# Performance work log

Hardware: AMD Instinct MI355X
Metric: run time of the kernel (lower is better)

Reference implementation:

```python
import jax, jax.numpy as jnp
import numpy as np

N = 8192       # number of points
C = 16         # num_colors (size of color distribution)
DIM = 2        # spatial dim (GeometricLoss(dim=2))


def setup_inputs() -> dict:
    key = jax.random.key(0)
    k1, k2 = jax.random.split(key)
    outputs = jax.random.normal(k1, (N, C), dtype=jnp.float32)
    points = jax.random.normal(k2, (N, DIM), dtype=jnp.float32)
    return {"outputs": outputs, "points": points, "k": 5}


def reference(outputs, points, k):
    # cdist(points, points) via the squared-norm expansion (avoids [N,N,dim] tensor)
    sq = jnp.sum(points * points, axis=1)                      # [N]
    d2 = sq[:, None] + sq[None, :] - 2.0 * (points @ points.T)  # [N,N]
    dist = jnp.sqrt(jnp.maximum(d2, 0.0))
    # k+1 smallest distances per row; drop self (distance 0)
    _, idx = jax.lax.top_k(-dist, k + 1)                        # [N,k+1]
    idx = idx[:, 1:]                                            # [N,k]
    neighbor_outputs = outputs[idx]                             # [N,k,C] gather
    # ||out_i - out_j|| over color dim, mean over all (i, neighbor) pairs
    differences = jnp.linalg.norm(outputs[:, None, :] - neighbor_outputs, axis=2)
    return differences.mean()
```

## Files before the change

### kernel.cpp

```cpp
#include <hip/hip_runtime.h>


static constexpr int NPTS = 8192;
static constexpr int KNN  = 5;
static constexpr int CH   = 16;
static constexpr int WPB  = 4;
static constexpr int NBLK = NPTS / WPB;
static constexpr int CAP  = 128;
static constexpr int NF4  = NPTS / 2;
static constexpr int BAT  = 8;
static constexpr int NBAT = NF4 / (64 * BAT);

__device__ __forceinline__ unsigned long long shfl_xor_u64(unsigned long long v, int m) {
    unsigned int lo = (unsigned int)v;
    unsigned int hi = (unsigned int)(v >> 32);
    lo = __shfl_xor(lo, m, 64);
    hi = __shfl_xor(hi, m, 64);
    return ((unsigned long long)hi << 32) | lo;
}

__global__ __launch_bounds__(256, 8) void knn_loss_kernel(
        const float* __restrict__ outputs,
        const float* __restrict__ points,
        float* __restrict__ partial) {
    const int wave = threadIdx.x >> 6;
    const int lane = threadIdx.x & 63;
    const int i = blockIdx.x * WPB + wave;

    const float2 pi = ((const float2*)points)[i];
    const float4* __restrict__ pts4 = (const float4*)points;
    const float FINF = __int_as_float(0x7f800000);

    float vA = FINF, vB = FINF;
    for (int b = 0; b < NBAT; ++b) {
        float4 p[BAT];
        #pragma unroll
        for (int q = 0; q < BAT; ++q)
            p[q] = pts4[b * (64 * BAT) + q * 64 + lane];
        #pragma unroll
        for (int q = 0; q < BAT; ++q) {
            const float dxa = pi.x - p[q].x, dya = pi.y - p[q].y;
            const float dxb = pi.x - p[q].z, dyb = pi.y - p[q].w;
            const float d2a = fmaf(dxa, dxa, dya * dya);
            const float d2b = fmaf(dxb, dxb, dyb * dyb);
            if (q & 1) vB = fminf(fminf(vB, d2a), d2b);
            else       vA = fminf(fminf(vA, d2a), d2b);
        }
    }

    float v = fmaxf(fminf(vA, vB), 0.0f);
    float T = 0.0f;
    #pragma unroll
    for (int t = 0; t < KNN + 1; ++t) {
        float m = v;
        #pragma unroll
        for (int d = 1; d < 64; d <<= 1) m = fminf(m, __shfl_xor(m, d, 64));
        if (v == m) v = FINF;
        T = m;
    }

    __shared__ unsigned long long buf[WPB][CAP];
    __shared__ int cnt[WPB];
    __shared__ float lds[WPB];
    if (lane == 0) cnt[wave] = 0;
    __syncthreads();

    for (int b = 0; b < NBAT; ++b) {
        float4 p[BAT];
        #pragma unroll
        for (int q = 0; q < BAT; ++q)
            p[q] = pts4[b * (64 * BAT) + q * 64 + lane];
        float bm = FINF;
        #pragma unroll
        for (int q = 0; q < BAT; ++q) {
            const float dxa = pi.x - p[q].x, dya = pi.y - p[q].y;
            const float dxb = pi.x - p[q].z, dyb = pi.y - p[q].w;
            const float d2a = fmaf(dxa, dxa, dya * dya);
            const float d2b = fmaf(dxb, dxb, dyb * dyb);
            bm = fminf(fminf(bm, d2a), d2b);
        }
        if (bm <= T) {
            #pragma unroll
            for (int q = 0; q < BAT; ++q) {
                const int it = b * (64 * BAT) + q * 64 + lane;
                const float dxa = pi.x - p[q].x, dya = pi.y - p[q].y;
                const float dxb = pi.x - p[q].z, dyb = pi.y - p[q].w;
                const float d2a = fmaf(dxa, dxa, dya * dya);
                const float d2b = fmaf(dxb, dxb, dyb * dyb);
                if (d2a <= T) {
                    const int pos = atomicAdd(&cnt[wave], 1);
                    if (pos < CAP)
                        buf[wave][pos] =
                            ((unsigned long long)__float_as_uint(fmaxf(d2a, 0.0f)) << 32)
                            | (unsigned int)(2 * it);
                }
                if (d2b <= T) {
                    const int pos = atomicAdd(&cnt[wave], 1);
                    if (pos < CAP)
                        buf[wave][pos] =
                            ((unsigned long long)__float_as_uint(fmaxf(d2b, 0.0f)) << 32)
                            | (unsigned int)(2 * it + 1);
                }
            }
        }
    }
    __syncthreads();

    const unsigned long long INF = ~0ull;
    const int n = min(cnt[wave], CAP);
    unsigned long long a = (lane      < n) ? buf[wave][lane]      : INF;
    unsigned long long b = (lane + 64 < n) ? buf[wave][lane + 64] : INF;
    if (b < a) { unsigned long long t = a; a = b; b = t; }

    unsigned int myj = 0;
    int active = 0;
    #pragma unroll
    for (int t = 0; t < KNN + 1; ++t) {
        unsigned long long m = a;
        #pragma unroll
        for (int d = 1; d < 64; d <<= 1) {
            const unsigned long long w = shfl_xor_u64(m, d);
            if (w < m) m = w;
        }
        if (a == m) { a = b; b = INF; }
        if (t >= 1 && lane == t) { myj = (unsigned int)m; active = 1; }
    }

    float nrm = 0.0f;
    if (active) {
        const float4* oi = (const float4*)(outputs + (size_t)i * CH);
        const float4* oj = (const float4*)(outputs + (size_t)myj * CH);
        float acc = 0.0f;
        #pragma unroll
        for (int q = 0; q < 4; ++q) {
            const float4 x = oi[q];
            const float4 y = oj[q];
            const float dx = x.x - y.x, dy = x.y - y.y;
            const float dz = x.z - y.z, dw = x.w - y.w;
            acc += dx * dx + dy * dy + dz * dz + dw * dw;
        }
        nrm = sqrtf(acc);
    }
    #pragma unroll
    for (int d = 1; d < 64; d <<= 1) nrm += __shfl_xor(nrm, d, 64);

    if (lane == 0) lds[wave] = nrm;
    __syncthreads();
    if (threadIdx.x == 0)
        partial[blockIdx.x] = lds[0] + lds[1] + lds[2] + lds[3];
}

__global__ __launch_bounds__(256) void finalize_kernel(
        const float* __restrict__ partial, float* __restrict__ out) {
    double s = 0.0;
    for (int idx = threadIdx.x; idx < NBLK; idx += 256) s += (double)partial[idx];
    #pragma unroll
    for (int d = 1; d < 64; d <<= 1) s += __shfl_xor(s, d, 64);
    __shared__ double lds[4];
    const int wave = threadIdx.x >> 6;
    const int lane = threadIdx.x & 63;
    if (lane == 0) lds[wave] = s;
    __syncthreads();
    if (threadIdx.x == 0)
        out[0] = (float)((lds[0] + lds[1] + lds[2] + lds[3]) /
                         (double)((long long)NPTS * KNN));
}

extern "C" void kernel_launch(void* const* d_in, const int* in_sizes, int n_in,
                              void* d_out, int out_size, void* d_ws, size_t ws_size,
                              hipStream_t stream) {
    const float* outputs = (const float*)d_in[0];
    const float* points  = (const float*)d_in[1];
    float* partial = (float*)d_ws;
    float* out = (float*)d_out;

    knn_loss_kernel<<<NBLK, 256, 0, stream>>>(outputs, points, partial);
    finalize_kernel<<<1, 256, 0, stream>>>(partial, out);
}
```

Measured before the change: 95.39 us.

## Process four query points per wave to reuse loaded candidate points

Each wave now handles four query points instead of one, so every candidate point loaded from memory is compared against four queries. Load traffic per query drops, the per-wave shuffle reductions are interleaved across the queries, and the grid shrinks by four. In exchange each lane keeps more registers, the occupancy hint drops from 8 to 4, and the second pass loses the per-batch early-exit check, so more threshold comparisons run on every batch.

```diff
diff --git a/kernel.cpp b/kernel.cpp
--- a/kernel.cpp
+++ b/kernel.cpp
@@ -1,15 +1,18 @@
 #include <hip/hip_runtime.h>
 
 
-static constexpr int NPTS = 8192;
-static constexpr int KNN  = 5;
-static constexpr int CH   = 16;
-static constexpr int WPB  = 4;
-static constexpr int NBLK = NPTS / WPB;
-static constexpr int CAP  = 128;
-static constexpr int NF4  = NPTS / 2;
-static constexpr int BAT  = 8;
-static constexpr int NBAT = NF4 / (64 * BAT);
+static constexpr int NPTS  = 8192;
+static constexpr int KNN   = 5;
+static constexpr int CH    = 16;
+static constexpr int WPB   = 4;
+static constexpr int QPW   = 4;
+static constexpr int NWAVE = NPTS / QPW;
+static constexpr int NBLK  = NWAVE / WPB;
+static constexpr int CAP   = 128;
+static constexpr int NF4   = NPTS / 2;
+static constexpr int BAT   = 4;
+static constexpr int NIT   = NF4 / 64;
+static constexpr int NB    = NIT / BAT;
 
 __device__ __forceinline__ unsigned long long shfl_xor_u64(unsigned long long v, int m) {
     unsigned int lo = (unsigned int)v;
@@ -19,135 +22,155 @@
     return ((unsigned long long)hi << 32) | lo;
 }
 
-__global__ __launch_bounds__(256, 8) void knn_loss_kernel(
+__global__ __launch_bounds__(256, 4) void knn_loss_kernel(
         const float* __restrict__ outputs,
         const float* __restrict__ points,
         float* __restrict__ partial) {
-    const int wave = threadIdx.x >> 6;
-    const int lane = threadIdx.x & 63;
-    const int i = blockIdx.x * WPB + wave;
-
-    const float2 pi = ((const float2*)points)[i];
+    const int wave  = threadIdx.x >> 6;
+    const int lane  = threadIdx.x & 63;
+    const int w     = blockIdx.x * WPB + wave;
+    const int qbase = w * QPW;
+
+    const float2* __restrict__ pts2 = (const float2*)points;
     const float4* __restrict__ pts4 = (const float4*)points;
     const float FINF = __int_as_float(0x7f800000);
 
-    float vA = FINF, vB = FINF;
-    for (int b = 0; b < NBAT; ++b) {
+    float pix[QPW], piy[QPW];
+    #pragma unroll
+    for (int q = 0; q < QPW; ++q) {
+        const float2 p = pts2[qbase + q];
+        pix[q] = p.x; piy[q] = p.y;
+    }
+
+    float acc[QPW];
+    #pragma unroll
+    for (int q = 0; q < QPW; ++q) acc[q] = FINF;
+
+    for (int b = 0; b < NB; ++b) {
         float4 p[BAT];
         #pragma unroll
-        for (int q = 0; q < BAT; ++q)
-            p[q] = pts4[b * (64 * BAT) + q * 64 + lane];
-        #pragma unroll
-        for (int q = 0; q < BAT; ++q) {
-            const float dxa = pi.x - p[q].x, dya = pi.y - p[q].y;
-            const float dxb = pi.x - p[q].z, dyb = pi.y - p[q].w;
-            const float d2a = fmaf(dxa, dxa, dya * dya);
-            const float d2b = fmaf(dxb, dxb, dyb * dyb);
-            if (q & 1) vB = fminf(fminf(vB, d2a), d2b);
-            else       vA = fminf(fminf(vA, d2a), d2b);
-        }
-    }
-
-    float v = fmaxf(fminf(vA, vB), 0.0f);
-    float T = 0.0f;
-    #pragma unroll
-    for (int t = 0; t < KNN + 1; ++t) {
-        float m = v;
-        #pragma unroll
-        for (int d = 1; d < 64; d <<= 1) m = fminf(m, __shfl_xor(m, d, 64));
-        if (v == m) v = FINF;
-        T = m;
-    }
-
-    __shared__ unsigned long long buf[WPB][CAP];
-    __shared__ int cnt[WPB];
-    __shared__ float lds[WPB];
-    if (lane == 0) cnt[wave] = 0;
-    __syncthreads();
-
-    for (int b = 0; b < NBAT; ++b) {
-        float4 p[BAT];
-        #pragma unroll
-        for (int q = 0; q < BAT; ++q)
-            p[q] = pts4[b * (64 * BAT) + q * 64 + lane];
-        float bm = FINF;
-        #pragma unroll
-        for (int q = 0; q < BAT; ++q) {
-            const float dxa = pi.x - p[q].x, dya = pi.y - p[q].y;
-            const float dxb = pi.x - p[q].z, dyb = pi.y - p[q].w;
-            const float d2a = fmaf(dxa, dxa, dya * dya);
-            const float d2b = fmaf(dxb, dxb, dyb * dyb);
-            bm = fminf(fminf(bm, d2a), d2b);
-        }
-        if (bm <= T) {
-            #pragma unroll
-            for (int q = 0; q < BAT; ++q) {
-                const int it = b * (64 * BAT) + q * 64 + lane;
-                const float dxa = pi.x - p[q].x, dya = pi.y - p[q].y;
-                const float dxb = pi.x - p[q].z, dyb = pi.y - p[q].w;
+        for (int u = 0; u < BAT; ++u)
+            p[u] = pts4[b * (BAT * 64) + u * 64 + lane];
+        #pragma unroll
+        for (int u = 0; u < BAT; ++u) {
+            #pragma unroll
+            for (int q = 0; q < QPW; ++q) {
+                const float dxa = pix[q] - p[u].x, dya = piy[q] - p[u].y;
+                const float dxb = pix[q] - p[u].z, dyb = piy[q] - p[u].w;
                 const float d2a = fmaf(dxa, dxa, dya * dya);
                 const float d2b = fmaf(dxb, dxb, dyb * dyb);
-                if (d2a <= T) {
-                    const int pos = atomicAdd(&cnt[wave], 1);
-                    if (pos < CAP)
-                        buf[wave][pos] =
-                            ((unsigned long long)__float_as_uint(fmaxf(d2a, 0.0f)) << 32)
-                            | (unsigned int)(2 * it);
+                acc[q] = fminf(fminf(acc[q], d2a), d2b);
+            }
+        }
+    }
+
+    float v[QPW], T[QPW];
+    #pragma unroll
+    for (int q = 0; q < QPW; ++q) v[q] = fmaxf(acc[q], 0.0f);
+    #pragma unroll
+    for (int t = 0; t < KNN + 1; ++t) {
+        float m[QPW];
+        #pragma unroll
+        for (int q = 0; q < QPW; ++q) m[q] = v[q];
+        #pragma unroll
+        for (int d = 1; d < 64; d <<= 1) {
+            #pragma unroll
+            for (int q = 0; q < QPW; ++q)
+                m[q] = fminf(m[q], __shfl_xor(m[q], d, 64));
+        }
+        #pragma unroll
+        for (int q = 0; q < QPW; ++q) {
+            if (v[q] == m[q]) v[q] = FINF;
+            T[q] = m[q];
+        }
+    }
+
+    __shared__ unsigned long long buf[WPB][QPW][CAP];
+    __shared__ int cnt[WPB][QPW];
+    __shared__ float red[WPB];
+    if (lane < QPW) cnt[wave][lane] = 0;
+    __syncthreads();
+
+    for (int b = 0; b < NB; ++b) {
+        float4 p[BAT];
+        #pragma unroll
+        for (int u = 0; u < BAT; ++u)
+            p[u] = pts4[b * (BAT * 64) + u * 64 + lane];
+        #pragma unroll
+        for (int u = 0; u < BAT; ++u) {
+            const int it = b * (BAT * 64) + u * 64 + lane;
+            #pragma unroll
+            for (int q = 0; q < QPW; ++q) {
+                const float dxa = pix[q] - p[u].x, dya = piy[q] - p[u].y;
+                const float dxb = pix[q] - p[u].z, dyb = piy[q] - p[u].w;
+                const float d2a = fmaf(dxa, dxa, dya * dya);
+                const float d2b = fmaf(dxb, dxb, dyb * dyb);
+                if (d2a <= T[q] || d2b <= T[q]) {
+                    if (d2a <= T[q]) {
+                        const int pos = atomicAdd(&cnt[wave][q], 1);
+                        if (pos < CAP)
+                            buf[wave][q][pos] =
+                                ((unsigned long long)__float_as_uint(fmaxf(d2a, 0.0f)) << 32)
+                                | (unsigned int)(2 * it);
+                    }
+                    if (d2b <= T[q]) {
+                        const int pos = atomicAdd(&cnt[wave][q], 1);
+                        if (pos < CAP)
+                            buf[wave][q][pos] =
+                                ((unsigned long long)__float_as_uint(fmaxf(d2b, 0.0f)) << 32)
+                                | (unsigned int)(2 * it + 1);
+                    }
                 }
-                if (d2b <= T) {
-                    const int pos = atomicAdd(&cnt[wave], 1);
-                    if (pos < CAP)
-                        buf[wave][pos] =
-                            ((unsigned long long)__float_as_uint(fmaxf(d2b, 0.0f)) << 32)
-                            | (unsigned int)(2 * it + 1);
-                }
-            }
-        }
-    }
-    __syncthreads();
-
-    const unsigned long long INF = ~0ull;
-    const int n = min(cnt[wave], CAP);
-    unsigned long long a = (lane      < n) ? buf[wave][lane]      : INF;
-    unsigned long long b = (lane + 64 < n) ? buf[wave][lane + 64] : INF;
-    if (b < a) { unsigned long long t = a; a = b; b = t; }
-
+            }
+        }
+    }
+    __syncthreads();
+
+    const unsigned long long INF64 = ~0ull;
     unsigned int myj = 0;
-    int active = 0;
-    #pragma unroll
-    for (int t = 0; t < KNN + 1; ++t) {
-        unsigned long long m = a;
-        #pragma unroll
-        for (int d = 1; d < 64; d <<= 1) {
-            const unsigned long long w = shfl_xor_u64(m, d);
-            if (w < m) m = w;
-        }
-        if (a == m) { a = b; b = INF; }
-        if (t >= 1 && lane == t) { myj = (unsigned int)m; active = 1; }
+    int myi = 0, active = 0;
+    #pragma unroll
+    for (int q = 0; q < QPW; ++q) {
+        const int n = min(cnt[wave][q], CAP);
+        unsigned long long a  = (lane      < n) ? buf[wave][q][lane]      : INF64;
+        unsigned long long b2 = (lane + 64 < n) ? buf[wave][q][lane + 64] : INF64;
+        if (b2 < a) { unsigned long long t = a; a = b2; b2 = t; }
+        #pragma unroll
+        for (int t = 0; t < KNN + 1; ++t) {
+            unsigned long long m = a;
+            #pragma unroll
+            for (int d = 1; d < 64; d <<= 1) {
+                const unsigned long long x = shfl_xor_u64(m, d);
+                if (x < m) m = x;
+            }
+            if (a == m) { a = b2; b2 = INF64; }
+            if (t >= 1 && lane == q * 8 + t) {
+                myj = (unsigned int)m; myi = qbase + q; active = 1;
+            }
+        }
     }
 
     float nrm = 0.0f;
     if (active) {
-        const float4* oi = (const float4*)(outputs + (size_t)i * CH);
+        const float4* oi = (const float4*)(outputs + (size_t)myi * CH);
         const float4* oj = (const float4*)(outputs + (size_t)myj * CH);
-        float acc = 0.0f;
-        #pragma unroll
-        for (int q = 0; q < 4; ++q) {
-            const float4 x = oi[q];
-            const float4 y = oj[q];
+        float s = 0.0f;
+        #pragma unroll
+        for (int c = 0; c < 4; ++c) {
+            const float4 x = oi[c], y = oj[c];
             const float dx = x.x - y.x, dy = x.y - y.y;
             const float dz = x.z - y.z, dw = x.w - y.w;
-            acc += dx * dx + dy * dy + dz * dz + dw * dw;
-        }
-        nrm = sqrtf(acc);
+            s += dx * dx + dy * dy + dz * dz + dw * dw;
+        }
+        nrm = sqrtf(s);
     }
     #pragma unroll
     for (int d = 1; d < 64; d <<= 1) nrm += __shfl_xor(nrm, d, 64);
 
-    if (lane == 0) lds[wave] = nrm;
+    if (lane == 0) red[wave] = nrm;
     __syncthreads();
     if (threadIdx.x == 0)
-        partial[blockIdx.x] = lds[0] + lds[1] + lds[2] + lds[3];
+        partial[blockIdx.x] = red[0] + red[1] + red[2] + red[3];
 }
 
 __global__ __launch_bounds__(256) void finalize_kernel(
```

Result: no change. 93.52 us (-2.0%).
